# Kernel optimization log

Hardware: AMD Instinct MI355X
Metric: run time of the kernel (lower is better)

Reference implementation:

```python
import jax, jax.numpy as jnp
import numpy as np
from jax import lax

B, H, W = 512, 128, 128
ARCH = [1, 4096, 4096, 4096, 4096]
CONV_THRESH = 0.0
GRAPH_THRESH = 0.8
EMBED_DIM = 1


def setup_inputs() -> dict:
    key = jax.random.key(0)
    ks = jax.random.split(key, 16)
    inp = {
        "x": jax.random.normal(ks[0], (B, 1, H, W), dtype=jnp.float32),
        "conv_w": jax.random.normal(ks[1], (1, 1, 2, 2), dtype=jnp.float32) * 0.5,
        "conv_b": jax.random.normal(ks[2], (1,), dtype=jnp.float32) * 0.1,
        "rotation": jax.random.normal(ks[3], (EMBED_DIM, EMBED_DIM), dtype=jnp.float32),
        "entangle": jax.random.normal(ks[4], (EMBED_DIM, EMBED_DIM), dtype=jnp.float32),
    }
    # Linear params, torch convention W: [out_f, in_f]
    for i, (fi, fo) in enumerate(zip(ARCH[:-1], ARCH[1:])):
        inp[f"W{i+1}"] = jax.random.normal(ks[5 + 2 * i], (fo, fi), dtype=jnp.float32) / np.sqrt(fi)
        inp[f"b{i+1}"] = jax.random.normal(ks[6 + 2 * i], (fo,), dtype=jnp.float32) * 0.01
    return inp


def _forward(x, conv_w, conv_b, rotation, entangle, W1, b1, W2, b2, W3, b3, W4, b4):
    # ConvFilter: 2x2 valid conv, sigmoid(logits - thresh), mean over C,H,W -> [B]
    logits = lax.conv_general_dilated(
        x, conv_w, window_strides=(1, 1), padding="VALID",
        dimension_numbers=("NCHW", "OIHW", "NCHW"))
    logits = logits + conv_b.reshape(1, -1, 1, 1)
    conv_out = jax.nn.sigmoid(logits - CONV_THRESH).mean(axis=(1, 2, 3))  # [B]
    conv_vec = conv_out[:, None]  # [B, 1] -> embed_dim forced to 1

    # ClassicalSelfAttention (embed_dim = 1)
    q = conv_vec @ rotation                      # [B, 1]
    k = conv_vec @ entangle                      # [B, 1]
    scores = jax.nn.softmax((q @ k.T) / np.sqrt(EMBED_DIM).astype(np.float32), axis=-1)  # [B, B]
    attn_out = scores @ conv_vec                 # [B, 1]

    # tanh MLP stack
    out = attn_out
    acts = []
    for Wl, bl in ((W1, b1), (W2, b2), (W3, b3), (W4, b4)):
        out = jnp.tanh(out @ Wl.T + bl)          # [B, out_f]
        acts.append(out)

    # Vectorized fidelity adjacency over equal-shaped layer activations:
    # normalized Gram matrix squared, thresholded (replaces the O(L^2)
    # Python loop with .item() syncs in the source).
    S = jnp.stack([a.reshape(-1) for a in acts])                  # [L, B*4096]
    S_hat = S / (jnp.linalg.norm(S, axis=1, keepdims=True) + 1e-12)
    fid = (S_hat @ S_hat.T) ** 2                                   # [L, L]
    L = len(acts)
    weights = jnp.where(fid >= GRAPH_THRESH, 1.0, 0.0) * (1.0 - jnp.eye(L, dtype=fid.dtype))
    return out, weights


def reference(x, conv_w, conv_b, rotation, entangle, W1, b1, W2, b2, W3, b3, W4, b4):
    return _forward(x, conv_w, conv_b, rotation, entangle, W1, b1, W2, b2, W3, b3, W4, b4)
```

## Files before the change

kernel.cpp:

```cpp
#include <hip/hip_runtime.h>
#include <cmath>


#define NEL (512 * 4096)

typedef float  floatx4 __attribute__((ext_vector_type(4)));
typedef _Float16 halfx8 __attribute__((ext_vector_type(8)));

#define BM 128
#define BN 128
#define BK 32
#define LDK 32

__global__ __launch_bounds__(256) void conv_mean_kernel(
    const float* __restrict__ x, const float* __restrict__ cw,
    const float* __restrict__ cb, float* __restrict__ c_out)
{
  __shared__ float sbuf[4];
  const int b = blockIdx.x;
  const float w00 = cw[0], w01 = cw[1], w10 = cw[2], w11 = cw[3];
  const float bias = cb[0];
  const float* xb = x + (size_t)b * 128 * 128;
  float acc = 0.f;
  for (int t = threadIdx.x; t < 127 * 32; t += 256) {
    const int i  = t >> 5;
    const int j0 = (t & 31) << 2;
    const float* pr0 = xb + i * 128 + j0;
    const float* pr1 = pr0 + 128;
    const float4 a4 = *reinterpret_cast<const float4*>(pr0);
    const float  a5 = pr0[4];
    const float4 b4 = *reinterpret_cast<const float4*>(pr1);
    const float  b5 = pr1[4];
    const float a[5] = {a4.x, a4.y, a4.z, a4.w, a5};
    const float bb[5] = {b4.x, b4.y, b4.z, b4.w, b5};
    #pragma unroll
    for (int m = 0; m < 4; ++m) {
      if (j0 + m < 127) {
        float v = w00 * a[m] + w01 * a[m + 1] + w10 * bb[m] + w11 * bb[m + 1] + bias;
        acc += 1.0f / (1.0f + __expf(-v));
      }
    }
  }
  #pragma unroll
  for (int off = 32; off > 0; off >>= 1) acc += __shfl_down(acc, off, 64);
  const int lane = threadIdx.x & 63, wv = threadIdx.x >> 6;
  if (lane == 0) sbuf[wv] = acc;
  __syncthreads();
  if (threadIdx.x == 0)
    c_out[b] = (sbuf[0] + sbuf[1] + sbuf[2] + sbuf[3]) * (1.0f / 16129.0f);
}

__global__ __launch_bounds__(256) void attn_layer1_kernel(
    const float* __restrict__ c, const float* __restrict__ rot,
    const float* __restrict__ ent, const float* __restrict__ W1,
    const float* __restrict__ b1, float* __restrict__ act1)
{
  __shared__ float sattn;
  const int i = blockIdx.x;
  if (threadIdx.x < 64) {
    const int lane = threadIdx.x;
    const float t = rot[0] * ent[0] * c[i];
    float vals[8], cj[8];
    float mx = -1e30f;
    #pragma unroll
    for (int u = 0; u < 8; ++u) {
      float cv = c[lane + u * 64];
      cj[u] = cv;
      vals[u] = t * cv;
      mx = fmaxf(mx, vals[u]);
    }
    #pragma unroll
    for (int off = 32; off > 0; off >>= 1) mx = fmaxf(mx, __shfl_down(mx, off, 64));
    mx = __shfl(mx, 0, 64);
    float se = 0.f, sw = 0.f;
    #pragma unroll
    for (int u = 0; u < 8; ++u) {
      float e = __expf(vals[u] - mx);
      se += e;
      sw += e * cj[u];
    }
    #pragma unroll
    for (int off = 32; off > 0; off >>= 1) {
      se += __shfl_down(se, off, 64);
      sw += __shfl_down(sw, off, 64);
    }
    if (lane == 0) sattn = sw / se;
  }
  __syncthreads();
  const float av = sattn;
  #pragma unroll
  for (int k = 0; k < 16; ++k) {
    const int o = k * 256 + threadIdx.x;
    act1[(size_t)i * 4096 + o] = tanhf(av * W1[o] + b1[o]);
  }
}

__global__ __launch_bounds__(256, 4) void gemm_kernel(
    const float* __restrict__ A, const float* __restrict__ W,
    float* __restrict__ part)
{
  __shared__ _Float16 As[2][BM][LDK];
  __shared__ _Float16 Ws[2][BN][LDK];
  const int K = 4096, N = 4096;
  const int tid  = threadIdx.x;
  const int lane = tid & 63;
  const int wave = tid >> 6;
  const int wm = (wave >> 1) * 64;
  const int wn = (wave & 1) * 64;
  const int q  = lane >> 4;
  const int ml = lane & 15;
  const int tileM = blockIdx.y * BM;
  const int tileN = blockIdx.x * BN;
  const int kbeg = blockIdx.z * 512;
  const int kend = kbeg + 512;
  float* Cb = part + (size_t)blockIdx.z * NEL;

  floatx4 acc[4][4] = {};

  const int r0 = tid >> 2;
  const int u0 = tid & 3;
  const int su0 = (u0 ^ (r0 & 3)) << 3;
  const int sq = (q ^ (ml & 3)) << 3;

  float4 pa[4], pw[4];
  auto load_tile = [&](int k0) {
    #pragma unroll
    for (int u = 0; u < 2; ++u) {
      const float* ap = A + (size_t)(tileM + r0 + u * 64) * K + k0 + u0 * 8;
      pa[2 * u]     = *reinterpret_cast<const float4*>(ap);
      pa[2 * u + 1] = *reinterpret_cast<const float4*>(ap + 4);
      const float* wp = W + (size_t)(tileN + r0 + u * 64) * K + k0 + u0 * 8;
      pw[2 * u]     = *reinterpret_cast<const float4*>(wp);
      pw[2 * u + 1] = *reinterpret_cast<const float4*>(wp + 4);
    }
  };
  auto store_tile = [&](int buf) {
    #pragma unroll
    for (int u = 0; u < 2; ++u) {
      halfx8 ha = { (_Float16)pa[2*u].x, (_Float16)pa[2*u].y,
                    (_Float16)pa[2*u].z, (_Float16)pa[2*u].w,
                    (_Float16)pa[2*u+1].x, (_Float16)pa[2*u+1].y,
                    (_Float16)pa[2*u+1].z, (_Float16)pa[2*u+1].w };
      *reinterpret_cast<halfx8*>(&As[buf][r0 + u * 64][su0]) = ha;
      halfx8 hw = { (_Float16)pw[2*u].x, (_Float16)pw[2*u].y,
                    (_Float16)pw[2*u].z, (_Float16)pw[2*u].w,
                    (_Float16)pw[2*u+1].x, (_Float16)pw[2*u+1].y,
                    (_Float16)pw[2*u+1].z, (_Float16)pw[2*u+1].w };
      *reinterpret_cast<halfx8*>(&Ws[buf][r0 + u * 64][su0]) = hw;
    }
  };

  load_tile(kbeg);
  store_tile(0);
  int cur = 0;

  for (int k0 = kbeg; k0 < kend; k0 += BK) {
    const bool more = (k0 + BK < kend);
    if (more) load_tile(k0 + BK);

    asm volatile("s_waitcnt lgkmcnt(0)" ::: "memory");
    __builtin_amdgcn_s_barrier();

    halfx8 af[4], bf[4];
    #pragma unroll
    for (int i = 0; i < 4; ++i)
      af[i] = *reinterpret_cast<const halfx8*>(&As[cur][wm + i * 16 + ml][sq]);
    #pragma unroll
    for (int j = 0; j < 4; ++j)
      bf[j] = *reinterpret_cast<const halfx8*>(&Ws[cur][wn + j * 16 + ml][sq]);

    #pragma unroll
    for (int i = 0; i < 4; ++i)
      #pragma unroll
      for (int j = 0; j < 4; ++j)
        acc[i][j] = __builtin_amdgcn_mfma_f32_16x16x32_f16(af[i], bf[j], acc[i][j], 0, 0, 0);

    if (more) store_tile(cur ^ 1);
    cur ^= 1;
  }

  #pragma unroll
  for (int i = 0; i < 4; ++i) {
    const int row0 = tileM + wm + i * 16 + q * 4;
    #pragma unroll
    for (int j = 0; j < 4; ++j) {
      const int col = tileN + wn + j * 16 + ml;
      #pragma unroll
      for (int r = 0; r < 4; ++r)
        Cb[(size_t)(row0 + r) * N + col] = acc[i][j][r];
    }
  }
}

__global__ __launch_bounds__(256) void combine_tanh_kernel(
    const float* __restrict__ part, const float* __restrict__ bias,
    float* __restrict__ outp)
{
  const int i4 = blockIdx.x * 256 + threadIdx.x;
  const floatx4* p4 = (const floatx4*)part;
  floatx4 s = p4[i4];
  #pragma unroll
  for (int z = 1; z < 8; ++z) s += p4[(size_t)z * (NEL / 4) + i4];
  const floatx4 bv = ((const floatx4*)bias)[i4 & 1023];
  floatx4 o;
  #pragma unroll
  for (int r = 0; r < 4; ++r) o[r] = tanhf(s[r] + bv[r]);
  ((floatx4*)outp)[i4] = o;
}

__global__ __launch_bounds__(256) void fid_dots_kernel(
    const float* __restrict__ a1, const float* __restrict__ a2,
    const float* __restrict__ a3, const float* __restrict__ a4,
    float* __restrict__ D)
{
  __shared__ float sred[4][10];
  float s[10] = {0, 0, 0, 0, 0, 0, 0, 0, 0, 0};
  const int n4 = NEL / 4;
  const int stride = gridDim.x * blockDim.x;
  const floatx4* p1 = (const floatx4*)a1;
  const floatx4* p2 = (const floatx4*)a2;
  const floatx4* p3 = (const floatx4*)a3;
  const floatx4* p4 = (const floatx4*)a4;
  for (int i = blockIdx.x * 256 + threadIdx.x; i < n4; i += stride) {
    floatx4 v1 = p1[i], v2 = p2[i], v3 = p3[i], v4 = p4[i];
    #pragma unroll
    for (int r = 0; r < 4; ++r) {
      s[0] += v1[r] * v1[r]; s[1] += v1[r] * v2[r]; s[2] += v1[r] * v3[r];
      s[3] += v1[r] * v4[r]; s[4] += v2[r] * v2[r]; s[5] += v2[r] * v3[r];
      s[6] += v2[r] * v4[r]; s[7] += v3[r] * v3[r]; s[8] += v3[r] * v4[r];
      s[9] += v4[r] * v4[r];
    }
  }
  const int lane = threadIdx.x & 63, wv = threadIdx.x >> 6;
  #pragma unroll
  for (int p = 0; p < 10; ++p) {
    float v = s[p];
    #pragma unroll
    for (int off = 32; off > 0; off >>= 1) v += __shfl_down(v, off, 64);
    if (lane == 0) sred[wv][p] = v;
  }
  __syncthreads();
  if (threadIdx.x < 10) {
    float v = sred[0][threadIdx.x] + sred[1][threadIdx.x] +
              sred[2][threadIdx.x] + sred[3][threadIdx.x];
    atomicAdd(&D[threadIdx.x * 16], v);
  }
}

__global__ void finalize_kernel(const float* __restrict__ D, float* __restrict__ wout)
{
  const int i = threadIdx.x;
  if (i >= 16) return;
  const int p = i >> 2, qq = i & 3;
  const int a = p < qq ? p : qq;
  const int b = p < qq ? qq : p;
  const int base[4] = {0, 4, 7, 9};
  const float dpq = D[(base[a] + (b - a)) * 16];
  const float npv = sqrtf(D[base[p] * 16]) + 1e-12f;
  const float nqv = sqrtf(D[base[qq] * 16]) + 1e-12f;
  const float ch = dpq / (npv * nqv);
  const float fid = ch * ch;
  wout[i] = (fid >= 0.8f && p != qq) ? 1.0f : 0.0f;
}

extern "C" void kernel_launch(void* const* d_in, const int* in_sizes, int n_in,
                              void* d_out, int out_size, void* d_ws, size_t ws_size,
                              hipStream_t stream)
{
  const float* x   = (const float*)d_in[0];
  const float* cw  = (const float*)d_in[1];
  const float* cb  = (const float*)d_in[2];
  const float* rot = (const float*)d_in[3];
  const float* ent = (const float*)d_in[4];
  const float* W1  = (const float*)d_in[5];
  const float* b1  = (const float*)d_in[6];
  const float* W2  = (const float*)d_in[7];
  const float* b2  = (const float*)d_in[8];
  const float* W3  = (const float*)d_in[9];
  const float* b3  = (const float*)d_in[10];
  const float* W4  = (const float*)d_in[11];
  const float* b4  = (const float*)d_in[12];
  float* out = (float*)d_out;

  char*  ws    = (char*)d_ws;
  float* c_buf = (float*)(ws + 0);
  float* D     = (float*)(ws + 4096);
  float* act1  = (float*)(ws + 8192);
  float* act2  = act1 + NEL;
  float* act3  = act2 + NEL;
  float* part  = act3 + NEL;
  float* wout  = out + NEL;

  hipMemsetAsync(D, 0, 10 * 16 * sizeof(float), stream);
  conv_mean_kernel<<<512, 256, 0, stream>>>(x, cw, cb, c_buf);
  attn_layer1_kernel<<<512, 256, 0, stream>>>(c_buf, rot, ent, W1, b1, act1);

  const int cgrid = NEL / 4 / 256;
  dim3 g(32, 4, 8);
  gemm_kernel<<<g, 256, 0, stream>>>(act1, W2, part);
  combine_tanh_kernel<<<cgrid, 256, 0, stream>>>(part, b2, act2);
  gemm_kernel<<<g, 256, 0, stream>>>(act2, W3, part);
  combine_tanh_kernel<<<cgrid, 256, 0, stream>>>(part, b3, act3);
  gemm_kernel<<<g, 256, 0, stream>>>(act3, W4, part);
  combine_tanh_kernel<<<cgrid, 256, 0, stream>>>(part, b4, out);

  fid_dots_kernel<<<256, 256, 0, stream>>>(act1, act2, act3, out, D);
  finalize_kernel<<<1, 64, 0, stream>>>(D, wout);
}
```

Measured before the change: 423.5 us.

## Pre-convert weights and activations to fp16 before split-K GEMMs

Adds a kernel that converts each 4096x4096 fp32 weight matrix to fp16 in a workspace buffer before its GEMM. Layer-1 and combine kernels now also write fp16 copies of the activations, so the GEMM reads half-width operands directly with no in-loop conversion. The shared-memory XOR swizzle is replaced by padding (LDK 40), and the memset is folded into the conv kernel. A workspace-size check falls back to split-K of 4. The cost is one extra full pass over each weight matrix every call plus the fp16 activation writes.

```diff
diff --git a/kernel.cpp b/kernel.cpp
--- a/kernel.cpp
+++ b/kernel.cpp
@@ -6,18 +6,21 @@
 
 typedef float  floatx4 __attribute__((ext_vector_type(4)));
 typedef _Float16 halfx8 __attribute__((ext_vector_type(8)));
+typedef _Float16 halfx4 __attribute__((ext_vector_type(4)));
 
 #define BM 128
 #define BN 128
 #define BK 32
-#define LDK 32
+#define LDK 40
 
 __global__ __launch_bounds__(256) void conv_mean_kernel(
     const float* __restrict__ x, const float* __restrict__ cw,
-    const float* __restrict__ cb, float* __restrict__ c_out)
+    const float* __restrict__ cb, float* __restrict__ c_out,
+    float* __restrict__ D)
 {
   __shared__ float sbuf[4];
   const int b = blockIdx.x;
+  if (b == 0 && threadIdx.x < 160) D[threadIdx.x] = 0.f;
   const float w00 = cw[0], w01 = cw[1], w10 = cw[2], w11 = cw[3];
   const float bias = cb[0];
   const float* xb = x + (size_t)b * 128 * 128;
@@ -53,7 +56,8 @@
 __global__ __launch_bounds__(256) void attn_layer1_kernel(
     const float* __restrict__ c, const float* __restrict__ rot,
     const float* __restrict__ ent, const float* __restrict__ W1,
-    const float* __restrict__ b1, float* __restrict__ act1)
+    const float* __restrict__ b1, float* __restrict__ act1,
+    _Float16* __restrict__ a1h)
 {
   __shared__ float sattn;
   const int i = blockIdx.x;
@@ -91,12 +95,29 @@
   #pragma unroll
   for (int k = 0; k < 16; ++k) {
     const int o = k * 256 + threadIdx.x;
-    act1[(size_t)i * 4096 + o] = tanhf(av * W1[o] + b1[o]);
+    const float v = tanhf(av * W1[o] + b1[o]);
+    act1[(size_t)i * 4096 + o] = v;
+    a1h[(size_t)i * 4096 + o] = (_Float16)v;
+  }
+}
+
+__global__ __launch_bounds__(256) void wconv_kernel(
+    const float* __restrict__ w, _Float16* __restrict__ wh)
+{
+  const int n8 = 4096 * 4096 / 8;
+  const int stride = gridDim.x * 256;
+  const float4* w4 = (const float4*)w;
+  for (int i = blockIdx.x * 256 + threadIdx.x; i < n8; i += stride) {
+    const float4 a = w4[2 * i];
+    const float4 b = w4[2 * i + 1];
+    halfx8 h = { (_Float16)a.x, (_Float16)a.y, (_Float16)a.z, (_Float16)a.w,
+                 (_Float16)b.x, (_Float16)b.y, (_Float16)b.z, (_Float16)b.w };
+    ((halfx8*)wh)[i] = h;
   }
 }
 
 __global__ __launch_bounds__(256, 4) void gemm_kernel(
-    const float* __restrict__ A, const float* __restrict__ W,
+    const _Float16* __restrict__ A16, const _Float16* __restrict__ W16,
     float* __restrict__ part)
 {
   __shared__ _Float16 As[2][BM][LDK];
@@ -111,42 +132,31 @@
   const int ml = lane & 15;
   const int tileM = blockIdx.y * BM;
   const int tileN = blockIdx.x * BN;
-  const int kbeg = blockIdx.z * 512;
-  const int kend = kbeg + 512;
+  const int Kslice = K / gridDim.z;
+  const int kbeg = blockIdx.z * Kslice;
+  const int kend = kbeg + Kslice;
   float* Cb = part + (size_t)blockIdx.z * NEL;
 
   floatx4 acc[4][4] = {};
 
-  const int r0 = tid >> 2;
-  const int u0 = tid & 3;
-  const int su0 = (u0 ^ (r0 & 3)) << 3;
-  const int sq = (q ^ (ml & 3)) << 3;
-
-  float4 pa[4], pw[4];
+  const int r0  = tid >> 2;
+  const int cc0 = (tid & 3) << 3;
+
+  halfx8 pa[2], pw[2];
   auto load_tile = [&](int k0) {
     #pragma unroll
     for (int u = 0; u < 2; ++u) {
-      const float* ap = A + (size_t)(tileM + r0 + u * 64) * K + k0 + u0 * 8;
-      pa[2 * u]     = *reinterpret_cast<const float4*>(ap);
-      pa[2 * u + 1] = *reinterpret_cast<const float4*>(ap + 4);
-      const float* wp = W + (size_t)(tileN + r0 + u * 64) * K + k0 + u0 * 8;
-      pw[2 * u]     = *reinterpret_cast<const float4*>(wp);
-      pw[2 * u + 1] = *reinterpret_cast<const float4*>(wp + 4);
+      pa[u] = *reinterpret_cast<const halfx8*>(
+          A16 + (size_t)(tileM + r0 + u * 64) * K + k0 + cc0);
+      pw[u] = *reinterpret_cast<const halfx8*>(
+          W16 + (size_t)(tileN + r0 + u * 64) * K + k0 + cc0);
     }
   };
   auto store_tile = [&](int buf) {
     #pragma unroll
     for (int u = 0; u < 2; ++u) {
-      halfx8 ha = { (_Float16)pa[2*u].x, (_Float16)pa[2*u].y,
-                    (_Float16)pa[2*u].z, (_Float16)pa[2*u].w,
-                    (_Float16)pa[2*u+1].x, (_Float16)pa[2*u+1].y,
-                    (_Float16)pa[2*u+1].z, (_Float16)pa[2*u+1].w };
-      *reinterpret_cast<halfx8*>(&As[buf][r0 + u * 64][su0]) = ha;
-      halfx8 hw = { (_Float16)pw[2*u].x, (_Float16)pw[2*u].y,
-                    (_Float16)pw[2*u].z, (_Float16)pw[2*u].w,
-                    (_Float16)pw[2*u+1].x, (_Float16)pw[2*u+1].y,
-                    (_Float16)pw[2*u+1].z, (_Float16)pw[2*u+1].w };
-      *reinterpret_cast<halfx8*>(&Ws[buf][r0 + u * 64][su0]) = hw;
+      *reinterpret_cast<halfx8*>(&As[buf][r0 + u * 64][cc0]) = pa[u];
+      *reinterpret_cast<halfx8*>(&Ws[buf][r0 + u * 64][cc0]) = pw[u];
     }
   };
 
@@ -164,10 +174,10 @@
     halfx8 af[4], bf[4];
     #pragma unroll
     for (int i = 0; i < 4; ++i)
-      af[i] = *reinterpret_cast<const halfx8*>(&As[cur][wm + i * 16 + ml][sq]);
+      af[i] = *reinterpret_cast<const halfx8*>(&As[cur][wm + i * 16 + ml][q * 8]);
     #pragma unroll
     for (int j = 0; j < 4; ++j)
-      bf[j] = *reinterpret_cast<const halfx8*>(&Ws[cur][wn + j * 16 + ml][sq]);
+      bf[j] = *reinterpret_cast<const halfx8*>(&Ws[cur][wn + j * 16 + ml][q * 8]);
 
     #pragma unroll
     for (int i = 0; i < 4; ++i)
@@ -192,20 +202,25 @@
   }
 }
 
+template<int S, bool H>
 __global__ __launch_bounds__(256) void combine_tanh_kernel(
     const float* __restrict__ part, const float* __restrict__ bias,
-    float* __restrict__ outp)
+    float* __restrict__ outp, _Float16* __restrict__ houtp)
 {
   const int i4 = blockIdx.x * 256 + threadIdx.x;
   const floatx4* p4 = (const floatx4*)part;
   floatx4 s = p4[i4];
   #pragma unroll
-  for (int z = 1; z < 8; ++z) s += p4[(size_t)z * (NEL / 4) + i4];
+  for (int z = 1; z < S; ++z) s += p4[(size_t)z * (NEL / 4) + i4];
   const floatx4 bv = ((const floatx4*)bias)[i4 & 1023];
   floatx4 o;
   #pragma unroll
   for (int r = 0; r < 4; ++r) o[r] = tanhf(s[r] + bv[r]);
   ((floatx4*)outp)[i4] = o;
+  if (H) {
+    halfx4 h = { (_Float16)o[0], (_Float16)o[1], (_Float16)o[2], (_Float16)o[3] };
+    ((halfx4*)houtp)[i4] = h;
+  }
 }
 
 __global__ __launch_bounds__(256) void fid_dots_kernel(
@@ -288,21 +303,44 @@
   float* act1  = (float*)(ws + 8192);
   float* act2  = act1 + NEL;
   float* act3  = act2 + NEL;
-  float* part  = act3 + NEL;
+  _Float16* a1h = (_Float16*)(act3 + NEL);
+  _Float16* a2h = a1h + NEL;
+  _Float16* a3h = a2h + NEL;
+  _Float16* wh  = a3h + NEL;
+  float* part  = (float*)(wh + (size_t)4096 * 4096);
   float* wout  = out + NEL;
 
-  hipMemsetAsync(D, 0, 10 * 16 * sizeof(float), stream);
-  conv_mean_kernel<<<512, 256, 0, stream>>>(x, cw, cb, c_buf);
-  attn_layer1_kernel<<<512, 256, 0, stream>>>(c_buf, rot, ent, W1, b1, act1);
+  const size_t base_need = 8192 + (size_t)3 * NEL * 4 + (size_t)3 * NEL * 2
+                         + (size_t)4096 * 4096 * 2;
+  const bool sk8 = ws_size >= base_need + (size_t)8 * NEL * 4;
+
+  conv_mean_kernel<<<512, 256, 0, stream>>>(x, cw, cb, c_buf, D);
+  attn_layer1_kernel<<<512, 256, 0, stream>>>(c_buf, rot, ent, W1, b1, act1, a1h);
 
   const int cgrid = NEL / 4 / 256;
-  dim3 g(32, 4, 8);
-  gemm_kernel<<<g, 256, 0, stream>>>(act1, W2, part);
-  combine_tanh_kernel<<<cgrid, 256, 0, stream>>>(part, b2, act2);
-  gemm_kernel<<<g, 256, 0, stream>>>(act2, W3, part);
-  combine_tanh_kernel<<<cgrid, 256, 0, stream>>>(part, b3, act3);
-  gemm_kernel<<<g, 256, 0, stream>>>(act3, W4, part);
-  combine_tanh_kernel<<<cgrid, 256, 0, stream>>>(part, b4, out);
+  if (sk8) {
+    dim3 g(32, 4, 8);
+    wconv_kernel<<<2048, 256, 0, stream>>>(W2, wh);
+    gemm_kernel<<<g, 256, 0, stream>>>(a1h, wh, part);
+    combine_tanh_kernel<8, true><<<cgrid, 256, 0, stream>>>(part, b2, act2, a2h);
+    wconv_kernel<<<2048, 256, 0, stream>>>(W3, wh);
+    gemm_kernel<<<g, 256, 0, stream>>>(a2h, wh, part);
+    combine_tanh_kernel<8, true><<<cgrid, 256, 0, stream>>>(part, b3, act3, a3h);
+    wconv_kernel<<<2048, 256, 0, stream>>>(W4, wh);
+    gemm_kernel<<<g, 256, 0, stream>>>(a3h, wh, part);
+    combine_tanh_kernel<8, false><<<cgrid, 256, 0, stream>>>(part, b4, out, nullptr);
+  } else {
+    dim3 g(32, 4, 4);
+    wconv_kernel<<<2048, 256, 0, stream>>>(W2, wh);
+    gemm_kernel<<<g, 256, 0, stream>>>(a1h, wh, part);
+    combine_tanh_kernel<4, true><<<cgrid, 256, 0, stream>>>(part, b2, act2, a2h);
+    wconv_kernel<<<2048, 256, 0, stream>>>(W3, wh);
+    gemm_kernel<<<g, 256, 0, stream>>>(a2h, wh, part);
+    combine_tanh_kernel<4, true><<<cgrid, 256, 0, stream>>>(part, b3, act3, a3h);
+    wconv_kernel<<<2048, 256, 0, stream>>>(W4, wh);
+    gemm_kernel<<<g, 256, 0, stream>>>(a3h, wh, part);
+    combine_tanh_kernel<4, false><<<cgrid, 256, 0, stream>>>(part, b4, out, nullptr);
+  }
 
   fid_dots_kernel<<<256, 256, 0, stream>>>(act1, act2, act3, out, D);
   finalize_kernel<<<1, 64, 0, stream>>>(D, wout);
```

Result: faster. 404.1 us (-4.6%).
